# Optimization experiments

Measured on AMD Instinct MI355X. Metric: run time of the kernel, lower is better.

The kernel has to match this reference:

```python
import jax, jax.numpy as jnp
import numpy as np

MAX_MARKER = 16


def setup_inputs() -> dict:
    key = jax.random.key(0)
    ks = jax.random.split(key, 7)
    B, W, H = 65536, 512, 8
    s1 = 1.0 / np.sqrt(W)
    s2 = 1.0 / np.sqrt(H)
    return {
        "x": jax.random.normal(ks[0], (B, W), dtype=jnp.float32),
        "W1": jax.random.uniform(ks[1], (H, W), jnp.float32, -s1, s1),
        "b1": jax.random.uniform(ks[2], (H,), jnp.float32, -s1, s1),
        "W2": jax.random.uniform(ks[3], (H, H), jnp.float32, -s2, s2),
        "b2": jax.random.uniform(ks[4], (H,), jnp.float32, -s2, s2),
        "W3": jax.random.uniform(ks[5], (W, H), jnp.float32, -s2, s2),
        "b3": jax.random.uniform(ks[6], (W,), jnp.float32, -s2, s2),
    }


def reference(x, W1, b1, W2, b2, W3, b3):
    # tiny MLP: window -> 8 -> 8 -> window
    h = jax.nn.relu(x @ W1.T + b1)
    h = jax.nn.relu(h @ W2.T + b2)
    y = h @ W3.T + b3
    p = jax.nn.softmax(y, axis=1)
    # force endpoints on (x.data[:,0]=1; x.data[:,-1]=1)
    p = p.at[:, 0].set(1.0).at[:, -1].set(1.0)
    # top-k along dim 1; threshold = min of the top-k values per row
    top_vals, _ = jax.lax.top_k(p, MAX_MARKER)
    thr = top_vals[:, -1:]  # sorted desc -> last is min, shape [B,1]
    # binary mask writes: >= thr -> 1, else 0
    return jnp.where(p >= thr, 1.0, 0.0).astype(p.dtype)
```

## Files before the change

### kernel.cpp

```cpp
#include <hip/hip_runtime.h>
#include <math.h>

#define B_ROWS 65536
#define WDIM 512
#define HDIM 8

typedef float native_float4 __attribute__((ext_vector_type(4)));

template<int CTRL, int ROWM>
__device__ __forceinline__ float dpp_mov(float oldv, float x) {
    return __int_as_float(__builtin_amdgcn_update_dpp(
        __float_as_int(oldv), __float_as_int(x), CTRL, ROWM, 0xF, false));
}

__device__ __forceinline__ float wave_sum(float x) {
    x += dpp_mov<0x121, 0xF>(0.f, x);
    x += dpp_mov<0x122, 0xF>(0.f, x);
    x += dpp_mov<0x124, 0xF>(0.f, x);
    x += dpp_mov<0x128, 0xF>(0.f, x);
    x += dpp_mov<0x142, 0xA>(0.f, x);
    x += dpp_mov<0x143, 0xC>(0.f, x);
    return __int_as_float(__builtin_amdgcn_readlane(__float_as_int(x), 63));
}

__device__ __forceinline__ float wave_max(float x) {
    x = fmaxf(x, dpp_mov<0x121, 0xF>(-INFINITY, x));
    x = fmaxf(x, dpp_mov<0x122, 0xF>(-INFINITY, x));
    x = fmaxf(x, dpp_mov<0x124, 0xF>(-INFINITY, x));
    x = fmaxf(x, dpp_mov<0x128, 0xF>(-INFINITY, x));
    x = fmaxf(x, dpp_mov<0x142, 0xA>(-INFINITY, x));
    x = fmaxf(x, dpp_mov<0x143, 0xC>(-INFINITY, x));
    return __int_as_float(__builtin_amdgcn_readlane(__float_as_int(x), 63));
}

__device__ __forceinline__ float dot8(native_float4 a0, native_float4 a1,
                                      native_float4 b0, native_float4 b1) {
    float s = a0.x * b0.x;
    s = fmaf(a0.y, b0.y, s); s = fmaf(a0.z, b0.z, s); s = fmaf(a0.w, b0.w, s);
    s = fmaf(a1.x, b1.x, s); s = fmaf(a1.y, b1.y, s);
    s = fmaf(a1.z, b1.z, s); s = fmaf(a1.w, b1.w, s);
    return s;
}

__global__ __launch_bounds__(256, 4)
void fused_mlp_topk(const float* __restrict__ x,
                    const float* __restrict__ W1,
                    const float* __restrict__ b1,
                    const float* __restrict__ W2,
                    const float* __restrict__ b2,
                    const float* __restrict__ W3,
                    const float* __restrict__ b3,
                    float* __restrict__ out)
{
    __shared__ __align__(16) float sW1[HDIM * WDIM];
    __shared__ __align__(16) float sW3t[HDIM * WDIM];
    __shared__ __align__(16) float sb3[WDIM];

    const int tid = threadIdx.x;
    for (int i = tid; i < HDIM * WDIM; i += 256) sW1[i] = W1[i];
    for (int i = tid; i < HDIM * WDIM; i += 256) {
        int r = i >> 3, k = i & 7;
        sW3t[k * WDIM + r] = W3[i];
    }
    for (int i = tid; i < WDIM; i += 256) sb3[i] = b3[i];
    __syncthreads();

    const int lane = tid & 63;
    const int wave_id = blockIdx.x * 4 + (tid >> 6);

    const native_float4* sW1v = reinterpret_cast<const native_float4*>(sW1);
    const native_float4* sW3v = reinterpret_cast<const native_float4*>(sW3t);
    const native_float4* sb3v = reinterpret_cast<const native_float4*>(sb3);

    int ra = wave_id * 2;
    const native_float4* xpa = reinterpret_cast<const native_float4*>(x + (size_t)ra * WDIM);
    const native_float4* xpb = xpa + (WDIM / 4);
    native_float4 xa0 = __builtin_nontemporal_load(xpa + lane);
    native_float4 xa1 = __builtin_nontemporal_load(xpa + lane + 64);
    native_float4 xb0 = __builtin_nontemporal_load(xpb + lane);
    native_float4 xb1 = __builtin_nontemporal_load(xpb + lane + 64);

    #pragma unroll 1
    for (int it = 0; it < 8; ++it) {
        float pa[HDIM], pb[HDIM];
        #pragma unroll
        for (int j = 0; j < HDIM; ++j) {
            native_float4 w0 = sW1v[j * 128 + lane];
            native_float4 w1 = sW1v[j * 128 + lane + 64];
            pa[j] = dot8(xa0, xa1, w0, w1);
            pb[j] = dot8(xb0, xb1, w0, w1);
        }
        float h1a[HDIM], h1b[HDIM];
        #pragma unroll
        for (int j = 0; j < HDIM; ++j) {
            float sa = wave_sum(pa[j]) + b1[j];
            float sb = wave_sum(pb[j]) + b1[j];
            h1a[j] = sa > 0.f ? sa : 0.f;
            h1b[j] = sb > 0.f ? sb : 0.f;
        }

        float h2a[HDIM], h2b[HDIM];
        #pragma unroll
        for (int j = 0; j < HDIM; ++j) {
            float va = b2[j], vb = b2[j];
            #pragma unroll
            for (int k = 0; k < HDIM; ++k) {
                const float w = W2[j * HDIM + k];
                va = fmaf(w, h1a[k], va);
                vb = fmaf(w, h1b[k], vb);
            }
            h2a[j] = va > 0.f ? va : 0.f;
            h2b[j] = vb > 0.f ? vb : 0.f;
        }

        native_float4 ya0 = sb3v[lane];
        native_float4 ya1 = sb3v[lane + 64];
        native_float4 yb0 = ya0, yb1 = ya1;
        #pragma unroll
        for (int k = 0; k < HDIM; ++k) {
            const float ha = h2a[k], hb = h2b[k];
            native_float4 w0 = sW3v[k * 128 + lane];
            native_float4 w1 = sW3v[k * 128 + lane + 64];
            ya0.x = fmaf(ha, w0.x, ya0.x); ya0.y = fmaf(ha, w0.y, ya0.y);
            ya0.z = fmaf(ha, w0.z, ya0.z); ya0.w = fmaf(ha, w0.w, ya0.w);
            ya1.x = fmaf(ha, w1.x, ya1.x); ya1.y = fmaf(ha, w1.y, ya1.y);
            ya1.z = fmaf(ha, w1.z, ya1.z); ya1.w = fmaf(ha, w1.w, ya1.w);
            yb0.x = fmaf(hb, w0.x, yb0.x); yb0.y = fmaf(hb, w0.y, yb0.y);
            yb0.z = fmaf(hb, w0.z, yb0.z); yb0.w = fmaf(hb, w0.w, yb0.w);
            yb1.x = fmaf(hb, w1.x, yb1.x); yb1.y = fmaf(hb, w1.y, yb1.y);
            yb1.z = fmaf(hb, w1.z, yb1.z); yb1.w = fmaf(hb, w1.w, yb1.w);
        }

        const int nra = ra + 8192;
        native_float4 nxa0, nxa1, nxb0, nxb1;
        if (it < 7) {
            const native_float4* nxpa = reinterpret_cast<const native_float4*>(x + (size_t)nra * WDIM);
            const native_float4* nxpb = nxpa + (WDIM / 4);
            nxa0 = __builtin_nontemporal_load(nxpa + lane);
            nxa1 = __builtin_nontemporal_load(nxpa + lane + 64);
            nxb0 = __builtin_nontemporal_load(nxpb + lane);
            nxb1 = __builtin_nontemporal_load(nxpb + lane + 64);
        }

        float lma = fmaxf(fmaxf(fmaxf(ya0.x, ya0.y), fmaxf(ya0.z, ya0.w)),
                          fmaxf(fmaxf(ya1.x, ya1.y), fmaxf(ya1.z, ya1.w)));
        float lmb = fmaxf(fmaxf(fmaxf(yb0.x, yb0.y), fmaxf(yb0.z, yb0.w)),
                          fmaxf(fmaxf(yb1.x, yb1.y), fmaxf(yb1.z, yb1.w)));
        float ma = wave_max(lma);
        float mb = wave_max(lmb);

        float ea[8], eb[8];
        ea[0] = expf(ya0.x - ma); ea[1] = expf(ya0.y - ma);
        ea[2] = expf(ya0.z - ma); ea[3] = expf(ya0.w - ma);
        ea[4] = expf(ya1.x - ma); ea[5] = expf(ya1.y - ma);
        ea[6] = expf(ya1.z - ma); ea[7] = expf(ya1.w - ma);
        eb[0] = expf(yb0.x - mb); eb[1] = expf(yb0.y - mb);
        eb[2] = expf(yb0.z - mb); eb[3] = expf(yb0.w - mb);
        eb[4] = expf(yb1.x - mb); eb[5] = expf(yb1.y - mb);
        eb[6] = expf(yb1.z - mb); eb[7] = expf(yb1.w - mb);
        float lsa = ((ea[0] + ea[1]) + (ea[2] + ea[3])) + ((ea[4] + ea[5]) + (ea[6] + ea[7]));
        float lsb = ((eb[0] + eb[1]) + (eb[2] + eb[3])) + ((eb[4] + eb[5]) + (eb[6] + eb[7]));
        float sa = wave_sum(lsa);
        float sb = wave_sum(lsb);

        float p_a[8], p_b[8];
        #pragma unroll
        for (int t = 0; t < 8; ++t) { p_a[t] = ea[t] / sa; p_b[t] = eb[t] / sb; }
        if (lane == 0)  { p_a[0] = 1.0f; p_b[0] = 1.0f; }
        if (lane == 63) { p_a[7] = 1.0f; p_b[7] = 1.0f; }

        unsigned Ua = 0x30000000u, Ub = 0x30000000u;
        for (int b = 27; b >= 0; --b) {
            const unsigned bit = 1u << b;
            const float cfa = __uint_as_float(Ua | bit);
            const float cfb = __uint_as_float(Ub | bit);
            int ca = 0, cb = 0;
            #pragma unroll
            for (int t = 0; t < 8; ++t) {
                ca += __popcll(__ballot(p_a[t] > cfa));
                cb += __popcll(__ballot(p_b[t] > cfb));
            }
            if (ca >= 16) Ua |= bit;
            if (cb >= 16) Ub |= bit;
        }
        const float thra = __uint_as_float(Ua + 1u);
        const float thrb = __uint_as_float(Ub + 1u);

        native_float4 r0, r1, q0, q1;
        r0.x = p_a[0] >= thra ? 1.f : 0.f;  r0.y = p_a[1] >= thra ? 1.f : 0.f;
        r0.z = p_a[2] >= thra ? 1.f : 0.f;  r0.w = p_a[3] >= thra ? 1.f : 0.f;
        r1.x = p_a[4] >= thra ? 1.f : 0.f;  r1.y = p_a[5] >= thra ? 1.f : 0.f;
        r1.z = p_a[6] >= thra ? 1.f : 0.f;  r1.w = p_a[7] >= thra ? 1.f : 0.f;
        q0.x = p_b[0] >= thrb ? 1.f : 0.f;  q0.y = p_b[1] >= thrb ? 1.f : 0.f;
        q0.z = p_b[2] >= thrb ? 1.f : 0.f;  q0.w = p_b[3] >= thrb ? 1.f : 0.f;
        q1.x = p_b[4] >= thrb ? 1.f : 0.f;  q1.y = p_b[5] >= thrb ? 1.f : 0.f;
        q1.z = p_b[6] >= thrb ? 1.f : 0.f;  q1.w = p_b[7] >= thrb ? 1.f : 0.f;

        native_float4* oa = reinterpret_cast<native_float4*>(out + (size_t)ra * WDIM);
        native_float4* ob = oa + (WDIM / 4);
        __builtin_nontemporal_store(r0, oa + lane);
        __builtin_nontemporal_store(r1, oa + lane + 64);
        __builtin_nontemporal_store(q0, ob + lane);
        __builtin_nontemporal_store(q1, ob + lane + 64);

        ra = nra;
        xa0 = nxa0; xa1 = nxa1; xb0 = nxb0; xb1 = nxb1;
    }
}

extern "C" void kernel_launch(void* const* d_in, const int* in_sizes, int n_in,
                              void* d_out, int out_size, void* d_ws, size_t ws_size,
                              hipStream_t stream) {
    const float* x  = (const float*)d_in[0];
    const float* W1 = (const float*)d_in[1];
    const float* b1 = (const float*)d_in[2];
    const float* W2 = (const float*)d_in[3];
    const float* b2 = (const float*)d_in[4];
    const float* W3 = (const float*)d_in[5];
    const float* b3 = (const float*)d_in[6];
    float* out = (float*)d_out;

    fused_mlp_topk<<<dim3(1024), dim3(256), 0, stream>>>(x, W1, b1, W2, b2, W3, b3, out);
}
```

Before: 354.5 us.

## Skip softmax by selecting top-k on monotone logit keys; retune grid

Softmax is monotone, so the top-k threshold is now found by a radix bit search over order-preserving integer keys of the raw logits. This drops the wave max, the exps, the sum reduction and the divides. The forced endpoints are excluded from the search by giving them key 0, the count target drops to 14, and they are set to 1 at output. The grid grows to 1280 blocks with launch bounds of 5 blocks per CU and a grid-stride loop, and b3 is read straight into registers instead of staged through LDS. Risks are ties in softmax output that differ from ties in the logits, and uneven work per wave from the grid-stride loop.

```diff
diff --git a/kernel.cpp b/kernel.cpp
--- a/kernel.cpp
+++ b/kernel.cpp
@@ -1,9 +1,9 @@
 #include <hip/hip_runtime.h>
 #include <math.h>
 
-#define B_ROWS 65536
 #define WDIM 512
 #define HDIM 8
+#define NPAIRS 32768
 
 typedef float native_float4 __attribute__((ext_vector_type(4)));
 
@@ -23,16 +23,6 @@
     return __int_as_float(__builtin_amdgcn_readlane(__float_as_int(x), 63));
 }
 
-__device__ __forceinline__ float wave_max(float x) {
-    x = fmaxf(x, dpp_mov<0x121, 0xF>(-INFINITY, x));
-    x = fmaxf(x, dpp_mov<0x122, 0xF>(-INFINITY, x));
-    x = fmaxf(x, dpp_mov<0x124, 0xF>(-INFINITY, x));
-    x = fmaxf(x, dpp_mov<0x128, 0xF>(-INFINITY, x));
-    x = fmaxf(x, dpp_mov<0x142, 0xA>(-INFINITY, x));
-    x = fmaxf(x, dpp_mov<0x143, 0xC>(-INFINITY, x));
-    return __int_as_float(__builtin_amdgcn_readlane(__float_as_int(x), 63));
-}
-
 __device__ __forceinline__ float dot8(native_float4 a0, native_float4 a1,
                                       native_float4 b0, native_float4 b1) {
     float s = a0.x * b0.x;
@@ -42,7 +32,12 @@
     return s;
 }
 
-__global__ __launch_bounds__(256, 4)
+__device__ __forceinline__ unsigned mono_key(float y) {
+    unsigned b = __float_as_uint(y);
+    return b ^ (unsigned)(((int)b >> 31) | (int)0x80000000);
+}
+
+__global__ __launch_bounds__(256, 5)
 void fused_mlp_topk(const float* __restrict__ x,
                     const float* __restrict__ W1,
                     const float* __restrict__ b1,
@@ -54,7 +49,6 @@
 {
     __shared__ __align__(16) float sW1[HDIM * WDIM];
     __shared__ __align__(16) float sW3t[HDIM * WDIM];
-    __shared__ __align__(16) float sb3[WDIM];
 
     const int tid = threadIdx.x;
     for (int i = tid; i < HDIM * WDIM; i += 256) sW1[i] = W1[i];
@@ -62,26 +56,28 @@
         int r = i >> 3, k = i & 7;
         sW3t[k * WDIM + r] = W3[i];
     }
-    for (int i = tid; i < WDIM; i += 256) sb3[i] = b3[i];
     __syncthreads();
 
     const int lane = tid & 63;
     const int wave_id = blockIdx.x * 4 + (tid >> 6);
+    const int n_waves = gridDim.x * 4;
 
     const native_float4* sW1v = reinterpret_cast<const native_float4*>(sW1);
     const native_float4* sW3v = reinterpret_cast<const native_float4*>(sW3t);
-    const native_float4* sb3v = reinterpret_cast<const native_float4*>(sb3);
-
-    int ra = wave_id * 2;
-    const native_float4* xpa = reinterpret_cast<const native_float4*>(x + (size_t)ra * WDIM);
-    const native_float4* xpb = xpa + (WDIM / 4);
+
+    const native_float4* b3v = reinterpret_cast<const native_float4*>(b3);
+    const native_float4 b3a = b3v[lane];
+    const native_float4 b3b = b3v[lane + 64];
+
+    int pair = wave_id;
+    const native_float4* xpa = reinterpret_cast<const native_float4*>(x + (size_t)pair * 2 * WDIM);
     native_float4 xa0 = __builtin_nontemporal_load(xpa + lane);
     native_float4 xa1 = __builtin_nontemporal_load(xpa + lane + 64);
-    native_float4 xb0 = __builtin_nontemporal_load(xpb + lane);
-    native_float4 xb1 = __builtin_nontemporal_load(xpb + lane + 64);
+    native_float4 xb0 = __builtin_nontemporal_load(xpa + lane + 128);
+    native_float4 xb1 = __builtin_nontemporal_load(xpa + lane + 192);
 
     #pragma unroll 1
-    for (int it = 0; it < 8; ++it) {
+    while (pair < NPAIRS) {
         float pa[HDIM], pb[HDIM];
         #pragma unroll
         for (int j = 0; j < HDIM; ++j) {
@@ -113,9 +109,8 @@
             h2b[j] = vb > 0.f ? vb : 0.f;
         }
 
-        native_float4 ya0 = sb3v[lane];
-        native_float4 ya1 = sb3v[lane + 64];
-        native_float4 yb0 = ya0, yb1 = ya1;
+        native_float4 ya0 = b3a, ya1 = b3b;
+        native_float4 yb0 = b3a, yb1 = b3b;
         #pragma unroll
         for (int k = 0; k < HDIM; ++k) {
             const float ha = h2a[k], hb = h2b[k];
@@ -131,79 +126,62 @@
             yb1.z = fmaf(hb, w1.z, yb1.z); yb1.w = fmaf(hb, w1.w, yb1.w);
         }
 
-        const int nra = ra + 8192;
+        const int npair = pair + n_waves;
         native_float4 nxa0, nxa1, nxb0, nxb1;
-        if (it < 7) {
-            const native_float4* nxpa = reinterpret_cast<const native_float4*>(x + (size_t)nra * WDIM);
-            const native_float4* nxpb = nxpa + (WDIM / 4);
-            nxa0 = __builtin_nontemporal_load(nxpa + lane);
-            nxa1 = __builtin_nontemporal_load(nxpa + lane + 64);
-            nxb0 = __builtin_nontemporal_load(nxpb + lane);
-            nxb1 = __builtin_nontemporal_load(nxpb + lane + 64);
-        }
-
-        float lma = fmaxf(fmaxf(fmaxf(ya0.x, ya0.y), fmaxf(ya0.z, ya0.w)),
-                          fmaxf(fmaxf(ya1.x, ya1.y), fmaxf(ya1.z, ya1.w)));
-        float lmb = fmaxf(fmaxf(fmaxf(yb0.x, yb0.y), fmaxf(yb0.z, yb0.w)),
-                          fmaxf(fmaxf(yb1.x, yb1.y), fmaxf(yb1.z, yb1.w)));
-        float ma = wave_max(lma);
-        float mb = wave_max(lmb);
-
-        float ea[8], eb[8];
-        ea[0] = expf(ya0.x - ma); ea[1] = expf(ya0.y - ma);
-        ea[2] = expf(ya0.z - ma); ea[3] = expf(ya0.w - ma);
-        ea[4] = expf(ya1.x - ma); ea[5] = expf(ya1.y - ma);
-        ea[6] = expf(ya1.z - ma); ea[7] = expf(ya1.w - ma);
-        eb[0] = expf(yb0.x - mb); eb[1] = expf(yb0.y - mb);
-        eb[2] = expf(yb0.z - mb); eb[3] = expf(yb0.w - mb);
-        eb[4] = expf(yb1.x - mb); eb[5] = expf(yb1.y - mb);
-        eb[6] = expf(yb1.z - mb); eb[7] = expf(yb1.w - mb);
-        float lsa = ((ea[0] + ea[1]) + (ea[2] + ea[3])) + ((ea[4] + ea[5]) + (ea[6] + ea[7]));
-        float lsb = ((eb[0] + eb[1]) + (eb[2] + eb[3])) + ((eb[4] + eb[5]) + (eb[6] + eb[7]));
-        float sa = wave_sum(lsa);
-        float sb = wave_sum(lsb);
-
-        float p_a[8], p_b[8];
-        #pragma unroll
-        for (int t = 0; t < 8; ++t) { p_a[t] = ea[t] / sa; p_b[t] = eb[t] / sb; }
-        if (lane == 0)  { p_a[0] = 1.0f; p_b[0] = 1.0f; }
-        if (lane == 63) { p_a[7] = 1.0f; p_b[7] = 1.0f; }
-
-        unsigned Ua = 0x30000000u, Ub = 0x30000000u;
-        for (int b = 27; b >= 0; --b) {
+        if (npair < NPAIRS) {
+            const native_float4* nxp = reinterpret_cast<const native_float4*>(x + (size_t)npair * 2 * WDIM);
+            nxa0 = __builtin_nontemporal_load(nxp + lane);
+            nxa1 = __builtin_nontemporal_load(nxp + lane + 64);
+            nxb0 = __builtin_nontemporal_load(nxp + lane + 128);
+            nxb1 = __builtin_nontemporal_load(nxp + lane + 192);
+        }
+
+        unsigned ka[8], kb[8];
+        ka[0] = mono_key(ya0.x); ka[1] = mono_key(ya0.y);
+        ka[2] = mono_key(ya0.z); ka[3] = mono_key(ya0.w);
+        ka[4] = mono_key(ya1.x); ka[5] = mono_key(ya1.y);
+        ka[6] = mono_key(ya1.z); ka[7] = mono_key(ya1.w);
+        kb[0] = mono_key(yb0.x); kb[1] = mono_key(yb0.y);
+        kb[2] = mono_key(yb0.z); kb[3] = mono_key(yb0.w);
+        kb[4] = mono_key(yb1.x); kb[5] = mono_key(yb1.y);
+        kb[6] = mono_key(yb1.z); kb[7] = mono_key(yb1.w);
+        if (lane == 0)  { ka[0] = 0u; kb[0] = 0u; }
+        if (lane == 63) { ka[7] = 0u; kb[7] = 0u; }
+
+        unsigned Ua = 0u, Ub = 0u;
+        for (int b = 31; b >= 0; --b) {
             const unsigned bit = 1u << b;
-            const float cfa = __uint_as_float(Ua | bit);
-            const float cfb = __uint_as_float(Ub | bit);
+            const unsigned cua = Ua | bit;
+            const unsigned cub = Ub | bit;
             int ca = 0, cb = 0;
             #pragma unroll
             for (int t = 0; t < 8; ++t) {
-                ca += __popcll(__ballot(p_a[t] > cfa));
-                cb += __popcll(__ballot(p_b[t] > cfb));
+                ca += __popcll(__ballot(ka[t] > cua));
+                cb += __popcll(__ballot(kb[t] > cub));
             }
-            if (ca >= 16) Ua |= bit;
-            if (cb >= 16) Ub |= bit;
-        }
-        const float thra = __uint_as_float(Ua + 1u);
-        const float thrb = __uint_as_float(Ub + 1u);
+            if (ca >= 14) Ua = cua;
+            if (cb >= 14) Ub = cub;
+        }
 
         native_float4 r0, r1, q0, q1;
-        r0.x = p_a[0] >= thra ? 1.f : 0.f;  r0.y = p_a[1] >= thra ? 1.f : 0.f;
-        r0.z = p_a[2] >= thra ? 1.f : 0.f;  r0.w = p_a[3] >= thra ? 1.f : 0.f;
-        r1.x = p_a[4] >= thra ? 1.f : 0.f;  r1.y = p_a[5] >= thra ? 1.f : 0.f;
-        r1.z = p_a[6] >= thra ? 1.f : 0.f;  r1.w = p_a[7] >= thra ? 1.f : 0.f;
-        q0.x = p_b[0] >= thrb ? 1.f : 0.f;  q0.y = p_b[1] >= thrb ? 1.f : 0.f;
-        q0.z = p_b[2] >= thrb ? 1.f : 0.f;  q0.w = p_b[3] >= thrb ? 1.f : 0.f;
-        q1.x = p_b[4] >= thrb ? 1.f : 0.f;  q1.y = p_b[5] >= thrb ? 1.f : 0.f;
-        q1.z = p_b[6] >= thrb ? 1.f : 0.f;  q1.w = p_b[7] >= thrb ? 1.f : 0.f;
-
-        native_float4* oa = reinterpret_cast<native_float4*>(out + (size_t)ra * WDIM);
-        native_float4* ob = oa + (WDIM / 4);
+        r0.x = ka[0] > Ua ? 1.f : 0.f;  r0.y = ka[1] > Ua ? 1.f : 0.f;
+        r0.z = ka[2] > Ua ? 1.f : 0.f;  r0.w = ka[3] > Ua ? 1.f : 0.f;
+        r1.x = ka[4] > Ua ? 1.f : 0.f;  r1.y = ka[5] > Ua ? 1.f : 0.f;
+        r1.z = ka[6] > Ua ? 1.f : 0.f;  r1.w = ka[7] > Ua ? 1.f : 0.f;
+        q0.x = kb[0] > Ub ? 1.f : 0.f;  q0.y = kb[1] > Ub ? 1.f : 0.f;
+        q0.z = kb[2] > Ub ? 1.f : 0.f;  q0.w = kb[3] > Ub ? 1.f : 0.f;
+        q1.x = kb[4] > Ub ? 1.f : 0.f;  q1.y = kb[5] > Ub ? 1.f : 0.f;
+        q1.z = kb[6] > Ub ? 1.f : 0.f;  q1.w = kb[7] > Ub ? 1.f : 0.f;
+        if (lane == 0)  { r0.x = 1.f; q0.x = 1.f; }
+        if (lane == 63) { r1.w = 1.f; q1.w = 1.f; }
+
+        native_float4* oa = reinterpret_cast<native_float4*>(out + (size_t)pair * 2 * WDIM);
         __builtin_nontemporal_store(r0, oa + lane);
         __builtin_nontemporal_store(r1, oa + lane + 64);
-        __builtin_nontemporal_store(q0, ob + lane);
-        __builtin_nontemporal_store(q1, ob + lane + 64);
-
-        ra = nra;
+        __builtin_nontemporal_store(q0, oa + lane + 128);
+        __builtin_nontemporal_store(q1, oa + lane + 192);
+
+        pair = npair;
         xa0 = nxa0; xa1 = nxa1; xb0 = nxb0; xb1 = nxb1;
     }
 }
@@ -220,5 +198,5 @@
     const float* b3 = (const float*)d_in[6];
     float* out = (float*)d_out;
 
-    fused_mlp_topk<<<dim3(1024), dim3(256), 0, stream>>>(x, W1, b1, W2, b2, W3, b3, out);
-}
+    fused_mlp_topk<<<dim3(1280), dim3(256), 0, stream>>>(x, W1, b1, W2, b2, W3, b3, out);
+}
```

After: 561.3 us. 1.58x slower.
